# Optimization experiments

Measured on AMD Instinct MI355X. Metric: run time of the kernel, lower is better.

Reference implementation:

```python
import jax, jax.numpy as jnp
import numpy as np

N = 50000      # nodes
E = 1600000    # edges (avg degree 32)
F_IN = 128
F_OUT = 64
ALPHA = 0.2    # LeakyReLU negative slope


def setup_inputs() -> dict:
    key = jax.random.key(0)
    ks = jax.random.split(key, 11)
    xav = 1.414 * (2.0 / (F_IN + F_OUT)) ** 0.5  # xavier_normal gain=1.414
    xav_a = 1.414 * (2.0 / (1 + 2 * F_OUT)) ** 0.5
    return {
        "input": jax.random.normal(ks[0], (N, F_IN), jnp.float32),
        "p_h": jax.random.normal(ks[1], (N, F_IN), jnp.float32),
        "new_h": jax.random.normal(ks[2], (N, F_IN), jnp.float32),
        "edge": jax.random.randint(ks[3], (2, E), 0, N),
        "edge_col": jax.random.randint(ks[4], (2, N), 0, N),
        "row_i": jax.random.randint(ks[5], (N,), 0, N),
        "row_resort": jax.random.randint(ks[6], (E,), 0, N),
        "adj": jnp.zeros((1,), jnp.float32),  # unused by forward (kept for signature parity)
        "W": jax.random.normal(ks[7], (F_IN, F_OUT), jnp.float32) * xav,
        "a1": jax.random.normal(ks[8], (1, 2 * F_OUT), jnp.float32) * xav_a,
        "a2": jax.random.normal(ks[9], (1, 2 * F_OUT), jnp.float32) * xav_a,
    }


def segment_softmax(src, index, num_segments):
    # torch_geometric.utils.softmax: numerically-stable softmax grouped by index
    m = jax.ops.segment_max(src, index, num_segments=num_segments)
    m = jnp.where(jnp.isfinite(m), m, 0.0)  # empty segments -> 0
    ex = jnp.exp(src - m[index])
    s = jax.ops.segment_sum(ex, index, num_segments=num_segments)
    return ex / (s[index] + 1e-16)


def reference(input, p_h, new_h, edge, edge_col, row_i, row_resort, adj, W, a1, a2):
    n = input.shape[0]
    fo = W.shape[1]
    h = input @ W            # [N, Fo]
    ph = p_h @ W             # [N, Fo]
    nh = new_h @ W           # [N, Fo]

    # a1 @ cat(h_src, p_h).T  ==  h_src @ a1_left + p_h @ a1_right  (avoids [E,2Fo] concat)
    a1l, a1r = a1[0, :fo], a1[0, fo:]
    col_score = h[edge_col[0]] @ a1l + ph @ a1r                 # [N]
    edge_col_e = jnp.exp(-jax.nn.leaky_relu(col_score, ALPHA))
    edge_col_e = segment_softmax(edge_col_e, row_i, n)

    a2l, a2r = a2[0, :fo], a2[0, fo:]
    row_score = nh[row_resort] @ a2l + h[edge[1]] @ a2r          # [E]
    edge_row_e = jnp.exp(-jax.nn.leaky_relu(row_score, ALPHA))

    edge_e = edge_row_e * edge_col_e[row_resort]                 # [E]

    # special_spmm(edge, edge_e, [N,N], ones) == segment row-sum
    e_rowsum = jax.ops.segment_sum(edge_e, edge[0], num_segments=n)[:, None]  # [N,1]
    e_rowsum = e_rowsum + jnp.where(e_rowsum == 0, 1.0, 0.0)

    attention_e = edge_e[:, None] / e_rowsum[edge[0]]            # [E,1]

    # dropout p=0.0 (eval): identity
    # special_spmm(edge, edge_e, [N,N], h) == segment-weighted aggregate
    h_prime = jax.ops.segment_sum(edge_e[:, None] * h[edge[1]], edge[0], num_segments=n)
    h_prime = h_prime / e_rowsum

    return jax.nn.elu(h_prime), edge, attention_e
```

## Files before the change

### kernel.cpp

```cpp
#include <hip/hip_runtime.h>

#define NN 50000
#define NE 1600000
#define FIN 128
#define FOUT 64
#define ALPHA 0.2f

#define RANGE 256
#define NB 196
#define EPB 2048

__global__ void k_sniff(const int* __restrict__ edge32, int* __restrict__ iflag) {
    __shared__ int zodd;
    if (threadIdx.x == 0) zodd = 0;
    __syncthreads();
    int z = 0;
    for (int i = threadIdx.x; i < 2048; i += 256)
        if (edge32[2 * i + 1] == 0) z++;
    atomicAdd(&zodd, z);
    __syncthreads();
    if (threadIdx.x == 0) *iflag = (zodd > 2000) ? 1 : 0;
}

__device__ inline int ldi(const void* p, size_t i, int isi64) {
    int v = isi64 ? (int)((const long long*)p)[i] : ((const int*)p)[i];
    return v < 0 ? 0 : (v >= NN ? NN - 1 : v);
}

__device__ inline unsigned short f2bf(float x) {
    unsigned u = __float_as_uint(x);
    return (unsigned short)((u + 0x7FFFu + ((u >> 16) & 1u)) >> 16);
}

__global__ void k_u(const float* __restrict__ W, const float* __restrict__ a1,
                    const float* __restrict__ a2, float* __restrict__ u) {
    int k = threadIdx.x;
    float u1 = 0.f, u2 = 0.f, u3 = 0.f, u4 = 0.f;
    for (int j = 0; j < FOUT; j++) {
        float w = W[k * FOUT + j];
        u1 += w * a1[j];
        u2 += w * a1[FOUT + j];
        u3 += w * a2[j];
        u4 += w * a2[FOUT + j];
    }
    u[k] = u1; u[128 + k] = u2; u[256 + k] = u3; u[384 + k] = u4;
}

__global__ __launch_bounds__(256) void k_gemm(const float* __restrict__ X,
                                              const float* __restrict__ W,
                                              unsigned short* __restrict__ h) {
    __shared__ float wlds[FIN * FOUT];
    __shared__ float xlds[4][4][FIN];
    int tid = threadIdx.x;
    for (int i = tid; i < FIN * FOUT; i += 256) wlds[i] = W[i];
    int wave = tid >> 6, lane = tid & 63;
    int base = blockIdx.x * 16 + wave * 4;
    for (int n0 = 0; n0 < 4; n0++) {
        float2 b = ((const float2*)(X + (size_t)(base + n0) * FIN))[lane];
        xlds[wave][n0][2 * lane] = b.x;
        xlds[wave][n0][2 * lane + 1] = b.y;
    }
    __syncthreads();
    float a0 = 0.f, a1v = 0.f, a2v = 0.f, a3 = 0.f;
    for (int k = 0; k < FIN; k++) {
        float w = wlds[k * FOUT + lane];
        a0  += xlds[wave][0][k] * w;
        a1v += xlds[wave][1][k] * w;
        a2v += xlds[wave][2][k] * w;
        a3  += xlds[wave][3][k] * w;
    }
    h[(size_t)(base + 0) * FOUT + lane] = f2bf(a0);
    h[(size_t)(base + 1) * FOUT + lane] = f2bf(a1v);
    h[(size_t)(base + 2) * FOUT + lane] = f2bf(a2v);
    h[(size_t)(base + 3) * FOUT + lane] = f2bf(a3);
}

__global__ __launch_bounds__(256) void k_svec(const float* __restrict__ input,
                                              const float* __restrict__ p_h,
                                              const float* __restrict__ new_h,
                                              const float* __restrict__ u,
                                              float* __restrict__ s1, float* __restrict__ s2,
                                              float* __restrict__ s3, float* __restrict__ s4) {
    int lane = threadIdx.x & 63;
    int v = blockIdx.x * 4 + (threadIdx.x >> 6);
    size_t row = (size_t)v * FIN;
    float2 bi = ((const float2*)(input + row))[lane];
    float2 bp = ((const float2*)(p_h   + row))[lane];
    float2 bn = ((const float2*)(new_h + row))[lane];
    float p1 = bi.x * u[2 * lane]       + bi.y * u[2 * lane + 1];
    float p2 = bp.x * u[128 + 2 * lane] + bp.y * u[128 + 2 * lane + 1];
    float p3 = bn.x * u[256 + 2 * lane] + bn.y * u[256 + 2 * lane + 1];
    float p4 = bi.x * u[384 + 2 * lane] + bi.y * u[384 + 2 * lane + 1];
#pragma unroll
    for (int off = 32; off > 0; off >>= 1) {
        p1 += __shfl_down(p1, off, 64);
        p2 += __shfl_down(p2, off, 64);
        p3 += __shfl_down(p3, off, 64);
        p4 += __shfl_down(p4, off, 64);
    }
    if (lane == 0) { s1[v] = p1; s2[v] = p2; s3[v] = p3; s4[v] = p4; }
}

__global__ void k_colscore(const float* __restrict__ s1, const float* __restrict__ s2,
                           const void* __restrict__ edge_col, const void* __restrict__ row_i,
                           const int* __restrict__ iflag,
                           float* __restrict__ ec, unsigned int* __restrict__ m) {
    int i = blockIdx.x * 256 + threadIdx.x;
    if (i >= NN) return;
    int i64 = *iflag;
    float cs = s1[ldi(edge_col, i, i64)] + s2[i];
    float l = cs > 0.f ? cs : ALPHA * cs;
    float e = expf(-l);
    ec[i] = e;
    atomicMax(&m[ldi(row_i, i, i64)], __float_as_uint(e));
}

__global__ void k_expsum(float* __restrict__ ec, const unsigned int* __restrict__ m,
                         const void* __restrict__ row_i, const int* __restrict__ iflag,
                         float* __restrict__ ssum) {
    int i = blockIdx.x * 256 + threadIdx.x;
    if (i >= NN) return;
    int r = ldi(row_i, i, *iflag);
    float e = expf(ec[i] - __uint_as_float(m[r]));
    ec[i] = e;
    atomicAdd(&ssum[r], e);
}

__global__ void k_norm(const float* __restrict__ ex, const float* __restrict__ ssum,
                       const void* __restrict__ row_i, const int* __restrict__ iflag,
                       float* __restrict__ ecs) {
    int i = blockIdx.x * 256 + threadIdx.x;
    if (i >= NN) return;
    ecs[i] = ex[i] / (ssum[ldi(row_i, i, *iflag)] + 1e-16f);
}

__global__ __launch_bounds__(512) void k_bhist(const void* __restrict__ edge,
                                               const int* __restrict__ iflag,
                                               int* __restrict__ bcnt) {
    __shared__ int hist[NB];
    int tid = threadIdx.x;
    for (int t = tid; t < NB; t += 512) hist[t] = 0;
    __syncthreads();
    int i64 = *iflag;
    int base = blockIdx.x * EPB;
#pragma unroll
    for (int k = 0; k < 4; k++) {
        int e = base + k * 512 + tid;
        if (e < NE) atomicAdd(&hist[ldi(edge, e, i64) >> 8], 1);
    }
    __syncthreads();
    for (int t = tid; t < NB; t += 512)
        if (hist[t]) atomicAdd(&bcnt[t], hist[t]);
}

__global__ __launch_bounds__(256) void k_bscan(const int* __restrict__ bcnt,
                                               int* __restrict__ bstart, int* __restrict__ bcur,
                                               int* __restrict__ start) {
    __shared__ int s[256];
    int tid = threadIdx.x;
    int x = (tid < NB) ? bcnt[tid] : 0;
    s[tid] = x;
    __syncthreads();
    for (int off = 1; off < 256; off <<= 1) {
        int t = (tid >= off) ? s[tid - off] : 0;
        __syncthreads();
        s[tid] += t;
        __syncthreads();
    }
    if (tid < NB) { int e = s[tid] - x; bstart[tid] = e; bcur[tid] = e; }
    if (tid == 0) { bstart[NB] = NE; start[NN] = NE; }
}

__global__ __launch_bounds__(512) void k_edgeA(const float* __restrict__ s3, const float* __restrict__ s4,
                                               const float* __restrict__ ecs,
                                               const void* __restrict__ edge, const void* __restrict__ row_resort,
                                               const int* __restrict__ iflag,
                                               int* __restrict__ bcur, uint2* __restrict__ tmp,
                                               float* __restrict__ edge_e ) {
    __shared__ int hist[NB];
    __shared__ int bbase[NB];
    int tid = threadIdx.x;
    for (int t = tid; t < NB; t += 512) hist[t] = 0;
    __syncthreads();
    int i64 = *iflag;
    int base = blockIdx.x * EPB;
    unsigned int key[4]; float val[4]; int rk[4], bk[4];
#pragma unroll
    for (int k = 0; k < 4; k++) {
        int e = base + k * 512 + tid;
        bk[k] = -1;
        if (e < NE) {
            int e0 = ldi(edge, e, i64);
            int e1 = ldi(edge, (size_t)NE + e, i64);
            int rr = ldi(row_resort, e, i64);
            float rs = s3[rr] + s4[e1];
            float l = rs > 0.f ? rs : ALPHA * rs;
            float ee = expf(-l) * ecs[rr];
            edge_e[e] = ee;
            key[k] = (unsigned int)e0 | ((unsigned int)e1 << 16);
            val[k] = ee;
            bk[k] = e0 >> 8;
            rk[k] = atomicAdd(&hist[bk[k]], 1);
        }
    }
    __syncthreads();
    for (int t = tid; t < NB; t += 512)
        bbase[t] = atomicAdd(&bcur[t], hist[t]);
    __syncthreads();
#pragma unroll
    for (int k = 0; k < 4; k++)
        if (bk[k] >= 0)
            tmp[bbase[bk[k]] + rk[k]] = make_uint2(key[k], __float_as_uint(val[k]));
}

__global__ __launch_bounds__(512) void k_edgeB(const uint2* __restrict__ tmp,
                                               const int* __restrict__ bstart,
                                               int* __restrict__ start,
                                               float2* __restrict__ pairs) {
    __shared__ int cnt[RANGE];
    __shared__ int s[RANGE];
    __shared__ int cur[RANGE];
    int b = blockIdx.x;
    int tid = threadIdx.x;
    int v0 = b * RANGE;
    if (tid < RANGE) cnt[tid] = 0;
    __syncthreads();
    int lo = bstart[b], hi = bstart[b + 1];
    for (int i = lo + tid; i < hi; i += 512)
        atomicAdd(&cnt[tmp[i].x & 0xFFu], 1);
    __syncthreads();
    if (tid < RANGE) s[tid] = cnt[tid];
    __syncthreads();
    for (int off = 1; off < RANGE; off <<= 1) {
        int t = 0;
        if (tid < RANGE && tid >= off) t = s[tid - off];
        __syncthreads();
        if (tid < RANGE) s[tid] += t;
        __syncthreads();
    }
    if (tid < RANGE) {
        int g = lo + s[tid] - cnt[tid];
        cur[tid] = g;
        int v = v0 + tid;
        if (v < NN) start[v] = g;
    }
    __syncthreads();
    for (int i = lo + tid; i < hi; i += 512) {
        uint2 r = tmp[i];
        int pos = atomicAdd(&cur[r.x & 0xFFu], 1);
        pairs[pos] = make_float2(__int_as_float((int)(r.x >> 16)), __uint_as_float(r.y));
    }
}

__global__ __launch_bounds__(256) void k_agg(const unsigned short* __restrict__ h,
                                             const float2* __restrict__ pairs,
                                             const int* __restrict__ start,
                                             float* __restrict__ ersum,
                                             float* __restrict__ out0) {
    int lane = threadIdx.x & 63;
    int half = lane >> 5;
    int fl   = lane & 31;
    int v = blockIdx.x * 4 + (threadIdx.x >> 6);
    int a = start[v], b = start[v + 1];
    float acc0 = 0.f, acc1 = 0.f, rs = 0.f;
    int j = a;
    for (; j + 4 <= b; j += 4) {
        float2 pA = pairs[j + half];
        float2 pB = pairs[j + 2 + half];
        unsigned hA = *(const unsigned*)(h + ((size_t)__float_as_int(pA.x) << 6) + 2 * fl);
        unsigned hB = *(const unsigned*)(h + ((size_t)__float_as_int(pB.x) << 6) + 2 * fl);
        acc0 += pA.y * __uint_as_float(hA << 16);
        acc1 += pA.y * __uint_as_float(hA & 0xFFFF0000u);
        acc0 += pB.y * __uint_as_float(hB << 16);
        acc1 += pB.y * __uint_as_float(hB & 0xFFFF0000u);
        rs += pA.y + pB.y;
    }
    for (; j < b; j += 2) {
        int e = j + half;
        float2 p = (e < b) ? pairs[e] : make_float2(__int_as_float(0), 0.f);
        unsigned hh = *(const unsigned*)(h + ((size_t)__float_as_int(p.x) << 6) + 2 * fl);
        acc0 += p.y * __uint_as_float(hh << 16);
        acc1 += p.y * __uint_as_float(hh & 0xFFFF0000u);
        rs += p.y;
    }
    acc0 += __shfl_xor(acc0, 32, 64);
    acc1 += __shfl_xor(acc1, 32, 64);
    rs   += __shfl_xor(rs, 32, 64);
    rs += (rs == 0.f) ? 1.f : 0.f;
    float hp0 = acc0 / rs, hp1 = acc1 / rs;
    hp0 = hp0 > 0.f ? hp0 : expm1f(hp0);
    hp1 = hp1 > 0.f ? hp1 : expm1f(hp1);
    if (half == 0) {
        ((float2*)(out0 + (size_t)v * FOUT))[fl] = make_float2(hp0, hp1);
        if (fl == 0) ersum[v] = rs;
    }
}

__global__ void k_att(const void* __restrict__ edge, const int* __restrict__ iflag,
                      const float* __restrict__ ersum, float* __restrict__ out2) {
    int e = blockIdx.x * 256 + threadIdx.x;
    out2[e] = out2[e] / ersum[ldi(edge, e, *iflag)];
}

__global__ void k_edgecopy(const void* __restrict__ edge, const int* __restrict__ iflag,
                           float* __restrict__ out1) {
    int i = blockIdx.x * 256 + threadIdx.x;
    int i64 = *iflag;
    int v = i64 ? (int)((const long long*)edge)[i] : ((const int*)edge)[i];
    out1[i] = (float)v;
}

extern "C" void kernel_launch(void* const* d_in, const int* in_sizes, int n_in,
                              void* d_out, int out_size, void* d_ws, size_t ws_size,
                              hipStream_t stream) {
    int ix[3] = {0, 1, 2}; int nx = 0;
    int iE = 3, iCol = 4, iRowI = 5, iRes = 6, iW = 8, iA1 = 9, iA2 = 10;
    bool a1seen = false;
    for (int i = 0; i < n_in; i++) {
        int s = in_sizes[i];
        if (s == NN * FIN) { if (nx < 3) ix[nx++] = i; }
        else if (s == 2 * NE) iE = i;
        else if (s == 2 * NN) iCol = i;
        else if (s == NN) iRowI = i;
        else if (s == NE) iRes = i;
        else if (s == FIN * FOUT) iW = i;
        else if (s == 2 * FOUT) { if (!a1seen) { iA1 = i; a1seen = true; } else iA2 = i; }
    }
    const float* input = (const float*)d_in[ix[0]];
    const float* p_h   = (const float*)d_in[ix[1]];
    const float* new_h = (const float*)d_in[ix[2]];
    const void* edge       = d_in[iE];
    const void* edge_col   = d_in[iCol];
    const void* row_i      = d_in[iRowI];
    const void* row_resort = d_in[iRes];
    const float* W  = (const float*)d_in[iW];
    const float* a1 = (const float*)d_in[iA1];
    const float* a2 = (const float*)d_in[iA2];

    float* out0 = (float*)d_out;
    float* out1 = out0 + (size_t)NN * FOUT;
    float* out2 = out1 + (size_t)2 * NE;

    uint2* tmp = (uint2*)out1;

    unsigned short* h = (unsigned short*)d_ws;
    float2* pairs  = (float2*)((float*)d_ws + (size_t)NN * FOUT);
    float*  s1     = (float*)(pairs + NE);
    float*  s2     = s1 + NN;
    float*  s3     = s2 + NN;
    float*  s4     = s3 + NN;
    float*  ec     = s4 + NN;
    float*  ecs    = ec + NN;
    float*  mseg   = ecs + NN;
    float*  ssum   = mseg + NN;
    int*    bcnt   = (int*)(ssum + NN);
    int*    start  = bcnt + NB;
    int*    bstart = start + NN + 1;
    int*    bcur   = bstart + NB + 1;
    float*  ersum  = (float*)(bcur + NB);
    float*  u      = ersum + NN;
    int*    iflag  = (int*)(u + 512);

    hipMemsetAsync(mseg, 0, ((size_t)2 * NN + NB) * sizeof(float), stream);

    k_sniff<<<1, 256, 0, stream>>>((const int*)edge, iflag);
    k_u<<<1, 128, 0, stream>>>(W, a1, a2, u);
    k_gemm<<<NN / 16, 256, 0, stream>>>(input, W, h);
    k_svec<<<NN / 4, 256, 0, stream>>>(input, p_h, new_h, u, s1, s2, s3, s4);
    k_colscore<<<(NN + 255) / 256, 256, 0, stream>>>(s1, s2, edge_col, row_i, iflag, ec, (unsigned int*)mseg);
    k_expsum<<<(NN + 255) / 256, 256, 0, stream>>>(ec, (const unsigned int*)mseg, row_i, iflag, ssum);
    k_norm<<<(NN + 255) / 256, 256, 0, stream>>>(ec, ssum, row_i, iflag, ecs);
    k_bhist<<<(NE + EPB - 1) / EPB, 512, 0, stream>>>(edge, iflag, bcnt);
    k_bscan<<<1, 256, 0, stream>>>(bcnt, bstart, bcur, start);
    k_edgeA<<<(NE + EPB - 1) / EPB, 512, 0, stream>>>(s3, s4, ecs, edge, row_resort, iflag, bcur, tmp, out2);
    k_edgeB<<<NB, 512, 0, stream>>>(tmp, bstart, start, pairs);
    k_agg<<<NN / 4, 256, 0, stream>>>(h, pairs, start, ersum, out0);
    k_att<<<NE / 256, 256, 0, stream>>>(edge, iflag, ersum, out2);
    k_edgecopy<<<2 * NE / 256, 256, 0, stream>>>(edge, iflag, out1);
}
```

Baseline: 338.3 us.

## Fuse bucket sort and aggregation into shared-memory atomic accumulation per bucket

Removes the second counting-sort pass (k_edgeB) and the CSR-based aggregation kernel. A new per-bucket kernel scans the coarsely bucketed edges and accumulates weighted neighbor features into a shared-memory tile of 128 rows x 65 floats with LDS atomics, then applies normalization and ELU. Buckets shrink to 128 nodes (391 blocks) so the tile fits in shared memory. The aim is to skip writing and re-reading the sorted pairs array and the start offsets. The cost is heavy LDS atomic contention, and with only 391 blocks of large shared memory the GPU may be under-occupied.

Result: slower. 968.4 us (+186.3%).

```diff
diff --git a/kernel.cpp b/kernel.cpp
--- a/kernel.cpp
+++ b/kernel.cpp
@@ -6,8 +6,8 @@
 #define FOUT 64
 #define ALPHA 0.2f
 
-#define RANGE 256
-#define NB 196
+#define RANGE 128
+#define NB 391
 #define EPB 2048
 
 __global__ void k_sniff(const int* __restrict__ edge32, int* __restrict__ iflag) {
@@ -146,29 +146,28 @@
 #pragma unroll
     for (int k = 0; k < 4; k++) {
         int e = base + k * 512 + tid;
-        if (e < NE) atomicAdd(&hist[ldi(edge, e, i64) >> 8], 1);
+        if (e < NE) atomicAdd(&hist[ldi(edge, e, i64) >> 7], 1);
     }
     __syncthreads();
     for (int t = tid; t < NB; t += 512)
         if (hist[t]) atomicAdd(&bcnt[t], hist[t]);
 }
 
-__global__ __launch_bounds__(256) void k_bscan(const int* __restrict__ bcnt,
-                                               int* __restrict__ bstart, int* __restrict__ bcur,
-                                               int* __restrict__ start) {
-    __shared__ int s[256];
+__global__ __launch_bounds__(512) void k_bscan(const int* __restrict__ bcnt,
+                                               int* __restrict__ bstart, int* __restrict__ bcur) {
+    __shared__ int s[512];
     int tid = threadIdx.x;
     int x = (tid < NB) ? bcnt[tid] : 0;
     s[tid] = x;
     __syncthreads();
-    for (int off = 1; off < 256; off <<= 1) {
+    for (int off = 1; off < 512; off <<= 1) {
         int t = (tid >= off) ? s[tid - off] : 0;
         __syncthreads();
         s[tid] += t;
         __syncthreads();
     }
     if (tid < NB) { int e = s[tid] - x; bstart[tid] = e; bcur[tid] = e; }
-    if (tid == 0) { bstart[NB] = NE; start[NN] = NE; }
+    if (tid == 0) bstart[NB] = NE;
 }
 
 __global__ __launch_bounds__(512) void k_edgeA(const float* __restrict__ s3, const float* __restrict__ s4,
@@ -199,7 +198,7 @@
             edge_e[e] = ee;
             key[k] = (unsigned int)e0 | ((unsigned int)e1 << 16);
             val[k] = ee;
-            bk[k] = e0 >> 8;
+            bk[k] = e0 >> 7;
             rk[k] = atomicAdd(&hist[bk[k]], 1);
         }
     }
@@ -213,86 +212,43 @@
             tmp[bbase[bk[k]] + rk[k]] = make_uint2(key[k], __float_as_uint(val[k]));
 }
 
-__global__ __launch_bounds__(512) void k_edgeB(const uint2* __restrict__ tmp,
-                                               const int* __restrict__ bstart,
-                                               int* __restrict__ start,
-                                               float2* __restrict__ pairs) {
-    __shared__ int cnt[RANGE];
-    __shared__ int s[RANGE];
-    __shared__ int cur[RANGE];
+__global__ __launch_bounds__(512) void k_bagg(const unsigned short* __restrict__ h,
+                                              const uint2* __restrict__ tmp,
+                                              const int* __restrict__ bstart,
+                                              float* __restrict__ ersum,
+                                              float* __restrict__ out0) {
+    __shared__ float lacc[RANGE * 65];
+    __shared__ float lrs[RANGE];
+    int tid = threadIdx.x;
     int b = blockIdx.x;
-    int tid = threadIdx.x;
     int v0 = b * RANGE;
-    if (tid < RANGE) cnt[tid] = 0;
+    for (int i = tid; i < RANGE * 65; i += 512) lacc[i] = 0.f;
+    if (tid < RANGE) lrs[tid] = 0.f;
     __syncthreads();
     int lo = bstart[b], hi = bstart[b + 1];
-    for (int i = lo + tid; i < hi; i += 512)
-        atomicAdd(&cnt[tmp[i].x & 0xFFu], 1);
-    __syncthreads();
-    if (tid < RANGE) s[tid] = cnt[tid];
-    __syncthreads();
-    for (int off = 1; off < RANGE; off <<= 1) {
-        int t = 0;
-        if (tid < RANGE && tid >= off) t = s[tid - off];
-        __syncthreads();
-        if (tid < RANGE) s[tid] += t;
-        __syncthreads();
-    }
-    if (tid < RANGE) {
-        int g = lo + s[tid] - cnt[tid];
-        cur[tid] = g;
-        int v = v0 + tid;
-        if (v < NN) start[v] = g;
-    }
-    __syncthreads();
-    for (int i = lo + tid; i < hi; i += 512) {
-        uint2 r = tmp[i];
-        int pos = atomicAdd(&cur[r.x & 0xFFu], 1);
-        pairs[pos] = make_float2(__int_as_float((int)(r.x >> 16)), __uint_as_float(r.y));
-    }
-}
-
-__global__ __launch_bounds__(256) void k_agg(const unsigned short* __restrict__ h,
-                                             const float2* __restrict__ pairs,
-                                             const int* __restrict__ start,
-                                             float* __restrict__ ersum,
-                                             float* __restrict__ out0) {
-    int lane = threadIdx.x & 63;
-    int half = lane >> 5;
-    int fl   = lane & 31;
-    int v = blockIdx.x * 4 + (threadIdx.x >> 6);
-    int a = start[v], b = start[v + 1];
-    float acc0 = 0.f, acc1 = 0.f, rs = 0.f;
-    int j = a;
-    for (; j + 4 <= b; j += 4) {
-        float2 pA = pairs[j + half];
-        float2 pB = pairs[j + 2 + half];
-        unsigned hA = *(const unsigned*)(h + ((size_t)__float_as_int(pA.x) << 6) + 2 * fl);
-        unsigned hB = *(const unsigned*)(h + ((size_t)__float_as_int(pB.x) << 6) + 2 * fl);
-        acc0 += pA.y * __uint_as_float(hA << 16);
-        acc1 += pA.y * __uint_as_float(hA & 0xFFFF0000u);
-        acc0 += pB.y * __uint_as_float(hB << 16);
-        acc1 += pB.y * __uint_as_float(hB & 0xFFFF0000u);
-        rs += pA.y + pB.y;
-    }
-    for (; j < b; j += 2) {
+    int lane = tid & 63, wid = tid >> 6;
+    int half = lane >> 5, fl = lane & 31;
+    for (int j = lo + wid * 2; j < hi; j += 16) {
         int e = j + half;
-        float2 p = (e < b) ? pairs[e] : make_float2(__int_as_float(0), 0.f);
-        unsigned hh = *(const unsigned*)(h + ((size_t)__float_as_int(p.x) << 6) + 2 * fl);
-        acc0 += p.y * __uint_as_float(hh << 16);
-        acc1 += p.y * __uint_as_float(hh & 0xFFFF0000u);
-        rs += p.y;
-    }
-    acc0 += __shfl_xor(acc0, 32, 64);
-    acc1 += __shfl_xor(acc1, 32, 64);
-    rs   += __shfl_xor(rs, 32, 64);
-    rs += (rs == 0.f) ? 1.f : 0.f;
-    float hp0 = acc0 / rs, hp1 = acc1 / rs;
-    hp0 = hp0 > 0.f ? hp0 : expm1f(hp0);
-    hp1 = hp1 > 0.f ? hp1 : expm1f(hp1);
-    if (half == 0) {
-        ((float2*)(out0 + (size_t)v * FOUT))[fl] = make_float2(hp0, hp1);
-        if (fl == 0) ersum[v] = rs;
+        uint2 r = (e < hi) ? tmp[e] : make_uint2(0u, 0u);
+        float ee = __uint_as_float(r.y);
+        int row = (int)(r.x & (RANGE - 1));
+        unsigned hh = *(const unsigned*)(h + (((size_t)(r.x >> 16)) << 6) + 2 * fl);
+        atomicAdd(&lacc[row * 65 + 2 * fl],     ee * __uint_as_float(hh << 16));
+        atomicAdd(&lacc[row * 65 + 2 * fl + 1], ee * __uint_as_float(hh & 0xFFFF0000u));
+        if (fl == 0) atomicAdd(&lrs[row], ee);
+    }
+    __syncthreads();
+    for (int i = tid; i < RANGE * FOUT; i += 512) {
+        int r = i >> 6, f = i & 63;
+        int v = v0 + r;
+        if (v < NN) {
+            float rs = lrs[r];
+            rs += (rs == 0.f) ? 1.f : 0.f;
+            float hp = lacc[r * 65 + f] / rs;
+            out0[(size_t)v * FOUT + f] = hp > 0.f ? hp : expm1f(hp);
+            if (f == 0) ersum[v] = rs;
+        }
     }
 }
 
@@ -344,8 +300,7 @@
     uint2* tmp = (uint2*)out1;
 
     unsigned short* h = (unsigned short*)d_ws;
-    float2* pairs  = (float2*)((float*)d_ws + (size_t)NN * FOUT);
-    float*  s1     = (float*)(pairs + NE);
+    float*  s1     = (float*)d_ws + (size_t)NN * FOUT / 2;
     float*  s2     = s1 + NN;
     float*  s3     = s2 + NN;
     float*  s4     = s3 + NN;
@@ -354,8 +309,7 @@
     float*  mseg   = ecs + NN;
     float*  ssum   = mseg + NN;
     int*    bcnt   = (int*)(ssum + NN);
-    int*    start  = bcnt + NB;
-    int*    bstart = start + NN + 1;
+    int*    bstart = bcnt + NB;
     int*    bcur   = bstart + NB + 1;
     float*  ersum  = (float*)(bcur + NB);
     float*  u      = ersum + NN;
@@ -371,10 +325,9 @@
     k_expsum<<<(NN + 255) / 256, 256, 0, stream>>>(ec, (const unsigned int*)mseg, row_i, iflag, ssum);
     k_norm<<<(NN + 255) / 256, 256, 0, stream>>>(ec, ssum, row_i, iflag, ecs);
     k_bhist<<<(NE + EPB - 1) / EPB, 512, 0, stream>>>(edge, iflag, bcnt);
-    k_bscan<<<1, 256, 0, stream>>>(bcnt, bstart, bcur, start);
+    k_bscan<<<1, 512, 0, stream>>>(bcnt, bstart, bcur);
     k_edgeA<<<(NE + EPB - 1) / EPB, 512, 0, stream>>>(s3, s4, ecs, edge, row_resort, iflag, bcur, tmp, out2);
-    k_edgeB<<<NB, 512, 0, stream>>>(tmp, bstart, start, pairs);
-    k_agg<<<NN / 4, 256, 0, stream>>>(h, pairs, start, ersum, out0);
+    k_bagg<<<NB, 512, 0, stream>>>(h, tmp, bstart, ersum, out0);
     k_att<<<NE / 256, 256, 0, stream>>>(edge, iflag, ersum, out2);
     k_edgecopy<<<2 * NE / 256, 256, 0, stream>>>(edge, iflag, out1);
 }
```

## Widen aggregation to 4-edge parallel lanes and fuse attention normalize with edge copy

Applied to the files above, without the earlier changes.

The aggregation kernel now splits each 64-lane wave into four groups of 16 lanes. Each lane loads 4 bf16 features with a uint2 load and processes 8 edges per iteration, using 8 waves per block. Partial sums are reduced with two xor-shuffle stages. The separate attention-normalize and edge-copy kernels are merged into one launch, which reuses the edge index read for both outputs and saves a launch and a second edge read. In exchange, each thread needs more registers, and the fused kernel clamps the node index and reads it through the first half of the edge array.

Result: faster. 330.5 us (-2.3%).

```diff
diff --git a/kernel.cpp b/kernel.cpp
--- a/kernel.cpp
+++ b/kernel.cpp
@@ -252,62 +252,65 @@
     }
 }
 
-__global__ __launch_bounds__(256) void k_agg(const unsigned short* __restrict__ h,
+__global__ __launch_bounds__(512) void k_agg(const unsigned short* __restrict__ h,
                                              const float2* __restrict__ pairs,
                                              const int* __restrict__ start,
                                              float* __restrict__ ersum,
                                              float* __restrict__ out0) {
     int lane = threadIdx.x & 63;
-    int half = lane >> 5;
-    int fl   = lane & 31;
-    int v = blockIdx.x * 4 + (threadIdx.x >> 6);
+    int q  = lane >> 4;
+    int fq = lane & 15;
+    int v = blockIdx.x * 8 + (threadIdx.x >> 6);
     int a = start[v], b = start[v + 1];
-    float acc0 = 0.f, acc1 = 0.f, rs = 0.f;
-    int j = a;
-    for (; j + 4 <= b; j += 4) {
-        float2 pA = pairs[j + half];
-        float2 pB = pairs[j + 2 + half];
-        unsigned hA = *(const unsigned*)(h + ((size_t)__float_as_int(pA.x) << 6) + 2 * fl);
-        unsigned hB = *(const unsigned*)(h + ((size_t)__float_as_int(pB.x) << 6) + 2 * fl);
-        acc0 += pA.y * __uint_as_float(hA << 16);
-        acc1 += pA.y * __uint_as_float(hA & 0xFFFF0000u);
-        acc0 += pB.y * __uint_as_float(hB << 16);
-        acc1 += pB.y * __uint_as_float(hB & 0xFFFF0000u);
+    float acc0 = 0.f, acc1 = 0.f, acc2 = 0.f, acc3 = 0.f, rs = 0.f;
+    for (int j = a; j < b; j += 8) {
+        int eA = j + q, eB = j + 4 + q;
+        float2 pA = (eA < b) ? pairs[eA] : make_float2(__int_as_float(0), 0.f);
+        float2 pB = (eB < b) ? pairs[eB] : make_float2(__int_as_float(0), 0.f);
+        uint2 hA = *(const uint2*)(h + (((size_t)__float_as_int(pA.x)) << 6) + 4 * fq);
+        uint2 hB = *(const uint2*)(h + (((size_t)__float_as_int(pB.x)) << 6) + 4 * fq);
+        acc0 += pA.y * __uint_as_float(hA.x << 16);
+        acc1 += pA.y * __uint_as_float(hA.x & 0xFFFF0000u);
+        acc2 += pA.y * __uint_as_float(hA.y << 16);
+        acc3 += pA.y * __uint_as_float(hA.y & 0xFFFF0000u);
+        acc0 += pB.y * __uint_as_float(hB.x << 16);
+        acc1 += pB.y * __uint_as_float(hB.x & 0xFFFF0000u);
+        acc2 += pB.y * __uint_as_float(hB.y << 16);
+        acc3 += pB.y * __uint_as_float(hB.y & 0xFFFF0000u);
         rs += pA.y + pB.y;
     }
-    for (; j < b; j += 2) {
-        int e = j + half;
-        float2 p = (e < b) ? pairs[e] : make_float2(__int_as_float(0), 0.f);
-        unsigned hh = *(const unsigned*)(h + ((size_t)__float_as_int(p.x) << 6) + 2 * fl);
-        acc0 += p.y * __uint_as_float(hh << 16);
-        acc1 += p.y * __uint_as_float(hh & 0xFFFF0000u);
-        rs += p.y;
-    }
-    acc0 += __shfl_xor(acc0, 32, 64);
-    acc1 += __shfl_xor(acc1, 32, 64);
-    rs   += __shfl_xor(rs, 32, 64);
-    rs += (rs == 0.f) ? 1.f : 0.f;
-    float hp0 = acc0 / rs, hp1 = acc1 / rs;
-    hp0 = hp0 > 0.f ? hp0 : expm1f(hp0);
-    hp1 = hp1 > 0.f ? hp1 : expm1f(hp1);
-    if (half == 0) {
-        ((float2*)(out0 + (size_t)v * FOUT))[fl] = make_float2(hp0, hp1);
-        if (fl == 0) ersum[v] = rs;
-    }
-}
-
-__global__ void k_att(const void* __restrict__ edge, const int* __restrict__ iflag,
-                      const float* __restrict__ ersum, float* __restrict__ out2) {
-    int e = blockIdx.x * 256 + threadIdx.x;
-    out2[e] = out2[e] / ersum[ldi(edge, e, *iflag)];
-}
-
-__global__ void k_edgecopy(const void* __restrict__ edge, const int* __restrict__ iflag,
-                           float* __restrict__ out1) {
+#pragma unroll
+    for (int off = 16; off <= 32; off <<= 1) {
+        acc0 += __shfl_xor(acc0, off, 64);
+        acc1 += __shfl_xor(acc1, off, 64);
+        acc2 += __shfl_xor(acc2, off, 64);
+        acc3 += __shfl_xor(acc3, off, 64);
+        rs   += __shfl_xor(rs, off, 64);
+    }
+    if (q == 0) {
+        rs += (rs == 0.f) ? 1.f : 0.f;
+        float4 o;
+        o.x = acc0 / rs; o.y = acc1 / rs; o.z = acc2 / rs; o.w = acc3 / rs;
+        o.x = o.x > 0.f ? o.x : expm1f(o.x);
+        o.y = o.y > 0.f ? o.y : expm1f(o.y);
+        o.z = o.z > 0.f ? o.z : expm1f(o.z);
+        o.w = o.w > 0.f ? o.w : expm1f(o.w);
+        ((float4*)(out0 + (size_t)v * FOUT))[fq] = o;
+        if (fq == 0) ersum[v] = rs;
+    }
+}
+
+__global__ __launch_bounds__(256) void k_final(const void* __restrict__ edge, const int* __restrict__ iflag,
+                                               const float* __restrict__ ersum,
+                                               float* __restrict__ out2, float* __restrict__ out1) {
     int i = blockIdx.x * 256 + threadIdx.x;
     int i64 = *iflag;
     int v = i64 ? (int)((const long long*)edge)[i] : ((const int*)edge)[i];
     out1[i] = (float)v;
+    if (i < NE) {
+        int e0 = v < 0 ? 0 : (v >= NN ? NN - 1 : v);
+        out2[i] = out2[i] / ersum[e0];
+    }
 }
 
 extern "C" void kernel_launch(void* const* d_in, const int* in_sizes, int n_in,
@@ -374,7 +377,6 @@
     k_bscan<<<1, 256, 0, stream>>>(bcnt, bstart, bcur, start);
     k_edgeA<<<(NE + EPB - 1) / EPB, 512, 0, stream>>>(s3, s4, ecs, edge, row_resort, iflag, bcur, tmp, out2);
     k_edgeB<<<NB, 512, 0, stream>>>(tmp, bstart, start, pairs);
-    k_agg<<<NN / 4, 256, 0, stream>>>(h, pairs, start, ersum, out0);
-    k_att<<<NE / 256, 256, 0, stream>>>(edge, iflag, ersum, out2);
-    k_edgecopy<<<2 * NE / 256, 256, 0, stream>>>(edge, iflag, out1);
-}
+    k_agg<<<NN / 8, 512, 0, stream>>>(h, pairs, start, ersum, out0);
+    k_final<<<2 * NE / 256, 256, 0, stream>>>(edge, iflag, ersum, out2, out1);
+}
```
